# Kernel optimization log

Hardware: AMD Instinct MI355X
Metric: run time of the kernel (lower is better)

The kernel has to match this reference:

```python
import jax, jax.numpy as jnp
import numpy as np

B, DIM, F, H = 16384, 64, 8, 8
D2 = DIM // 2


def setup_inputs() -> dict:
    key = jax.random.key(0)
    ks = jax.random.split(key, 8)
    s = 0.1  # small init so exp(s_net) stays well-conditioned
    return {
        "x": jax.random.normal(ks[0], (B, DIM), jnp.float32),
        "x_star": jax.random.normal(ks[1], (B, DIM), jnp.float32),
        "W0": jax.random.normal(ks[2], (F, 4, H, D2), jnp.float32) * s,
        "b0": jax.random.normal(ks[3], (F, 4, H), jnp.float32) * s,
        "W1": jax.random.normal(ks[4], (F, 4, H, H), jnp.float32) * s,
        "b1": jax.random.normal(ks[5], (F, 4, H), jnp.float32) * s,
        "W2": jax.random.normal(ks[6], (F, 4, D2, H), jnp.float32) * s,
        "b2": jax.random.normal(ks[7], (F, 4, D2), jnp.float32) * s,
    }


def _fcnn(v, w0, c0, w1, c1, w2, c2):
    # FCNN: Linear -> Tanh -> Linear -> Tanh -> Linear, on a single vector v [D2]
    h = jnp.tanh(w0 @ v + c0)
    h = jnp.tanh(w1 @ h + c1)
    return w2 @ h + c2


def _phi(v, params):
    # Chain of n_flows RealNVP coupling layers on a single sample v [DIM].
    def step(v, p):
        W0, b0, W1, b1, W2, b2 = p  # leading axis 4 = (t1, s1, t2, s2)
        lo, up = v[:D2], v[D2:]
        t1 = _fcnn(lo, W0[0], b0[0], W1[0], b1[0], W2[0], b2[0])
        s1 = _fcnn(lo, W0[1], b0[1], W1[1], b1[1], W2[1], b2[1])
        up = t1 + up * jnp.exp(s1)
        t2 = _fcnn(up, W0[2], b0[2], W1[2], b1[2], W2[2], b2[2])
        s2 = _fcnn(up, W0[3], b0[3], W1[3], b1[3], W2[3], b2[3])
        lo = t2 + lo * jnp.exp(s2)
        return jnp.concatenate([lo, up]), None

    z, _ = jax.lax.scan(step, v, params)
    return z


def reference(x, x_star, W0, b0, W1, b1, W2, b2):
    params = (W0, b0, W1, b1, W2, b2)
    # Per-sample Jacobian of the flow (replaces torch autograd loop): [B, DIM, DIM]
    jac = jax.vmap(jax.jacfwd(lambda v: _phi(v, params)))(x)
    # -grad of quadratic potential (feature=None): -2 * (x - x_star)
    g = -2.0 * (x - x_star)
    # torch.solve(potential_grad, phi_jac): solve J u = g per sample
    return jnp.linalg.solve(jac, g[..., None])[..., 0]
```

## Files before the change

kernel.cpp:

```cpp
#include <hip/hip_runtime.h>


namespace {

typedef __fp16 f16x2 __attribute__((ext_vector_type(2)));
typedef __fp16 v4h __attribute__((ext_vector_type(4)));
typedef __fp16 v8h __attribute__((ext_vector_type(8)));
typedef float f32x4 __attribute__((ext_vector_type(4)));

constexpr int NB = 16384;

__device__ __forceinline__ float frcp(float x) { return __builtin_amdgcn_rcpf(x); }
__device__ __forceinline__ float ftanh(float x) {
  float e = __expf(2.f * x);
  return 1.f - 2.f * frcp(e + 1.f);
}
__device__ __forceinline__ f16x2 pk(float a, float b) {
  return __builtin_amdgcn_cvt_pkrtz(a, b);
}

union U8 { v8h v; f16x2 h[4]; };
union U4 { v4h v; f16x2 h[2]; };

__device__ __forceinline__ int pbase(int p) {
  return ((p >> 1) << 2) + ((p & 1) << 1);
}

template <bool JVP>
__device__ __forceinline__ void pair_apply(
    const f16x2* __restrict__ LW0, const f16x2* __restrict__ LW1,
    const f16x2* __restrict__ LW2, const float* __restrict__ LB0,
    const float* __restrict__ LB1, const float* __restrict__ LB2, int p,
    int n, int q, const float v[8], const float* __restrict__ u, float t8[8],
    float s8[8], float* __restrict__ ut8, float* __restrict__ us8) {
  v4h z4;
#pragma unroll
  for (int jj = 0; jj < 4; ++jj) z4[jj] = (__fp16)0.f;
  const f32x4 zc = {0.f, 0.f, 0.f, 0.f};

  U8 B;
  B.h[0] = pk(v[0], v[1]);
  B.h[1] = pk(v[2], v[3]);
  B.h[2] = pk(v[4], v[5]);
  B.h[3] = pk(v[6], v[7]);

  const v8h A0 = *(const v8h*)(LW0 + ((p * 64 + q * 16 + n) << 2));
  const f32x4 c0 = *(const f32x4*)(LB0 + p * 16 + q * 4);
  f32x4 d1 = __builtin_amdgcn_mfma_f32_16x16x32_f16(A0, B.v, c0, 0, 0, 0);
  float h1[4];
#pragma unroll
  for (int r = 0; r < 4; ++r) h1[r] = ftanh(d1[r]);
  U4 H1;
  H1.h[0] = pk(h1[0], h1[1]);
  H1.h[1] = pk(h1[2], h1[3]);

  const bool act1 = (n < 8) == (q < 2);
  v4h A1 = *(const v4h*)(LW1 + (p * 64 + ((n & 7) << 2) + ((q & 1) << 1) +
                                ((n >= 8) ? 32 : 0)));
  A1 = act1 ? A1 : z4;
  const f32x4 c1 = *(const f32x4*)(LB1 + p * 16 + q * 4);
  f32x4 d2 = __builtin_amdgcn_mfma_f32_16x16x16f16(A1, H1.v, c1, 0, 0, 0);
  float h2[4];
#pragma unroll
  for (int r = 0; r < 4; ++r) h2[r] = ftanh(d2[r]);
  U4 H2;
  H2.h[0] = pk(h2[0], h2[1]);
  H2.h[1] = pk(h2[2], h2[3]);

  U4 G2;
  if constexpr (JVP) {
    U8 Bu;
    Bu.h[0] = pk(u[0], u[1]);
    Bu.h[1] = pk(u[2], u[3]);
    Bu.h[2] = pk(u[4], u[5]);
    Bu.h[3] = pk(u[6], u[7]);
    f32x4 d1u = __builtin_amdgcn_mfma_f32_16x16x32_f16(A0, Bu.v, zc, 0, 0, 0);
    float g1[4];
#pragma unroll
    for (int r = 0; r < 4; ++r) g1[r] = (1.f - h1[r] * h1[r]) * d1u[r];
    U4 G1;
    G1.h[0] = pk(g1[0], g1[1]);
    G1.h[1] = pk(g1[2], g1[3]);
    f32x4 d2u = __builtin_amdgcn_mfma_f32_16x16x16f16(A1, G1.v, zc, 0, 0, 0);
    float g2[4];
#pragma unroll
    for (int r = 0; r < 4; ++r) g2[r] = (1.f - h2[r] * h2[r]) * d2u[r];
    G2.h[0] = pk(g2[0], g2[1]);
    G2.h[1] = pk(g2[2], g2[3]);
  }

#pragma unroll
  for (int b = 0; b < 4; ++b) {
    const bool act = (b < 2) == (q < 2);
    v4h Ab = *(const v4h*)(LW2 + (p * 256 + b * 64 + n * 4 + ((q & 1) << 1)));
    Ab = act ? Ab : z4;
    const f32x4 cb = *(const f32x4*)(LB2 + (p * 4 + b) * 16 + q * 4);
    f32x4 ob = __builtin_amdgcn_mfma_f32_16x16x16f16(Ab, H2.v, cb, 0, 0, 0);
    float* dst = (b < 2) ? t8 : s8;
    const int off = (b & 1) * 4;
#pragma unroll
    for (int r = 0; r < 4; ++r) dst[off + r] = ob[r];
    if constexpr (JVP) {
      f32x4 jb = __builtin_amdgcn_mfma_f32_16x16x16f16(Ab, G2.v, zc, 0, 0, 0);
      float* jdst = (b < 2) ? ut8 : us8;
#pragma unroll
      for (int r = 0; r < 4; ++r) jdst[off + r] = jb[r];
    }
  }
}

}

__global__ __launch_bounds__(256, 1) void nf_policy_kernel(
    const float* __restrict__ x, const float* __restrict__ xs,
    const float* __restrict__ gW0, const float* __restrict__ gb0,
    const float* __restrict__ gW1, const float* __restrict__ gb1,
    const float* __restrict__ gW2, const float* __restrict__ gb2,
    float* __restrict__ out) {
  __shared__ __align__(16) f16x2 LW0[4096];
  __shared__ __align__(16) f16x2 LW1[1024];
  __shared__ __align__(16) f16x2 LW2[4096];
  __shared__ __align__(16) float LB0[256];
  __shared__ __align__(16) float LB1[256];
  __shared__ __align__(16) float LB2[1024];

  const int tid = threadIdx.x;
  for (int i = tid; i < 4096; i += 256) {
    const int p = i >> 8, rem = i & 255, q = rem >> 6, rem2 = rem & 63;
    const int mm = rem2 >> 2, w = rem2 & 3;
    const int net = pbase(p) + (mm >> 3);
    const int h = mm & 7, k0 = q * 8 + w * 2;
    const float* src = gW0 + net * 256 + h * 32 + k0;
    LW0[i] = pk(src[0], src[1]);
  }
  for (int i = tid; i < 1024; i += 256) {
    const int p = i >> 6, rem = i & 63, half = rem >> 5;
    const int row = (rem >> 2) & 7, kk = rem & 3;
    const int net = pbase(p) + half;
    const float* src = gW1 + net * 64 + row * 8 + kk * 2;
    LW1[i] = pk(src[0], src[1]);
  }
  for (int i = tid; i < 4096; i += 256) {
    const int p = i >> 8, rem = i & 255, b = rem >> 6, rem2 = rem & 63;
    const int mm = rem2 >> 2, kk = rem2 & 3;
    const int net = pbase(p) + (b >> 1);
    const int d = 8 * (mm >> 2) + ((b & 1) << 2) + (mm & 3);
    const float* src = gW2 + net * 256 + d * 8 + kk * 2;
    LW2[i] = pk(src[0], src[1]);
  }
  for (int i = tid; i < 256; i += 256) {
    const int p = i >> 4, mm = i & 15;
    const int net = pbase(p) + (mm >> 3);
    LB0[i] = gb0[net * 8 + (mm & 7)];
    LB1[i] = gb1[net * 8 + (mm & 7)];
  }
  for (int i = tid; i < 1024; i += 256) {
    const int p = i >> 6, b = (i >> 4) & 3, mm = i & 15;
    const int net = pbase(p) + (b >> 1);
    const int d = 8 * (mm >> 2) + ((b & 1) << 2) + (mm & 3);
    LB2[i] = gb2[net * 32 + d];
  }
  __syncthreads();

  const int lane = tid & 63;
  const int wv = tid >> 6;
  const int n = lane & 15;
  const int q = lane >> 4;
  const int e = blockIdx.x * 64 + wv * 16 + n;

  float lo[8], up[8], av[8], bv[8];
  {
    const float* xe = x + (size_t)e * 64;
    const float* se = xs + (size_t)e * 64;
    const float4 a0 = *(const float4*)(xe + q * 8);
    const float4 a1 = *(const float4*)(xe + q * 8 + 4);
    const float4 u0 = *(const float4*)(xe + 32 + q * 8);
    const float4 u1 = *(const float4*)(xe + 32 + q * 8 + 4);
    const float4 p0 = *(const float4*)(se + q * 8);
    const float4 p1 = *(const float4*)(se + q * 8 + 4);
    const float4 r0 = *(const float4*)(se + 32 + q * 8);
    const float4 r1 = *(const float4*)(se + 32 + q * 8 + 4);
    lo[0] = a0.x; lo[1] = a0.y; lo[2] = a0.z; lo[3] = a0.w;
    lo[4] = a1.x; lo[5] = a1.y; lo[6] = a1.z; lo[7] = a1.w;
    up[0] = u0.x; up[1] = u0.y; up[2] = u0.z; up[3] = u0.w;
    up[4] = u1.x; up[5] = u1.y; up[6] = u1.z; up[7] = u1.w;
    av[0] = -2.f * (a0.x - p0.x); av[1] = -2.f * (a0.y - p0.y);
    av[2] = -2.f * (a0.z - p0.z); av[3] = -2.f * (a0.w - p0.w);
    av[4] = -2.f * (a1.x - p1.x); av[5] = -2.f * (a1.y - p1.y);
    av[6] = -2.f * (a1.z - p1.z); av[7] = -2.f * (a1.w - p1.w);
    bv[0] = -2.f * (u0.x - r0.x); bv[1] = -2.f * (u0.y - r0.y);
    bv[2] = -2.f * (u0.z - r0.z); bv[3] = -2.f * (u0.w - r0.w);
    bv[4] = -2.f * (u1.x - r1.x); bv[5] = -2.f * (u1.y - r1.y);
    bv[6] = -2.f * (u1.z - r1.z); bv[7] = -2.f * (u1.w - r1.w);
  }

  float t8[8], s8[8], ut8[8], us8[8];

#pragma unroll 1
  for (int i = 0; i < 8; ++i) {
    pair_apply<false>(LW0, LW1, LW2, LB0, LB1, LB2, 2 * i, n, q, lo, nullptr,
                      t8, s8, nullptr, nullptr);
#pragma unroll
    for (int j = 0; j < 8; ++j) up[j] = fmaf(up[j], __expf(s8[j]), t8[j]);
    pair_apply<false>(LW0, LW1, LW2, LB0, LB1, LB2, 2 * i + 1, n, q, up,
                      nullptr, t8, s8, nullptr, nullptr);
#pragma unroll
    for (int j = 0; j < 8; ++j) lo[j] = fmaf(lo[j], __expf(s8[j]), t8[j]);
  }

#pragma unroll 1
  for (int i = 7; i >= 0; --i) {
    pair_apply<true>(LW0, LW1, LW2, LB0, LB1, LB2, 2 * i + 1, n, q, up, bv,
                     t8, s8, ut8, us8);
#pragma unroll
    for (int j = 0; j < 8; ++j) {
      const float esi = __expf(-s8[j]);
      const float d = lo[j] - t8[j];
      lo[j] = d * esi;
      av[j] = (av[j] - ut8[j] - d * us8[j]) * esi;
    }
    pair_apply<true>(LW0, LW1, LW2, LB0, LB1, LB2, 2 * i, n, q, lo, av, t8,
                     s8, ut8, us8);
#pragma unroll
    for (int j = 0; j < 8; ++j) {
      const float esi = __expf(-s8[j]);
      const float d = up[j] - t8[j];
      up[j] = d * esi;
      bv[j] = (bv[j] - ut8[j] - d * us8[j]) * esi;
    }
  }

  {
    float* oe = out + (size_t)e * 64;
    float4 v;
    v.x = av[0]; v.y = av[1]; v.z = av[2]; v.w = av[3];
    *(float4*)(oe + q * 8) = v;
    v.x = av[4]; v.y = av[5]; v.z = av[6]; v.w = av[7];
    *(float4*)(oe + q * 8 + 4) = v;
    v.x = bv[0]; v.y = bv[1]; v.z = bv[2]; v.w = bv[3];
    *(float4*)(oe + 32 + q * 8) = v;
    v.x = bv[4]; v.y = bv[5]; v.z = bv[6]; v.w = bv[7];
    *(float4*)(oe + 32 + q * 8 + 4) = v;
  }
}

extern "C" void kernel_launch(void* const* d_in, const int* in_sizes, int n_in,
                              void* d_out, int out_size, void* d_ws,
                              size_t ws_size, hipStream_t stream) {
  const float* x  = (const float*)d_in[0];
  const float* xs = (const float*)d_in[1];
  const float* W0 = (const float*)d_in[2];
  const float* b0 = (const float*)d_in[3];
  const float* W1 = (const float*)d_in[4];
  const float* b1 = (const float*)d_in[5];
  const float* W2 = (const float*)d_in[6];
  const float* b2 = (const float*)d_in[7];
  float* out = (float*)d_out;

  dim3 grid(NB / 64);
  dim3 block(256);
  nf_policy_kernel<<<grid, block, 0, stream>>>(x, xs, W0, b0, W1, b1, W2, b2,
                                               out);
}
```

Baseline: 95.45 us.

## Cache forward hidden activations in LDS to skip recomputation in backward pass

```diff
diff --git a/kernel.cpp b/kernel.cpp
--- a/kernel.cpp
+++ b/kernel.cpp
@@ -19,94 +19,11 @@
   return __builtin_amdgcn_cvt_pkrtz(a, b);
 }
 
-union U8 { v8h v; f16x2 h[4]; };
-union U4 { v4h v; f16x2 h[2]; };
+union U8 { v8h v; f16x2 h[4]; float4 f4; };
+union U4 { v4h v; f16x2 h[2]; float2 f2; };
 
 __device__ __forceinline__ int pbase(int p) {
   return ((p >> 1) << 2) + ((p & 1) << 1);
-}
-
-template <bool JVP>
-__device__ __forceinline__ void pair_apply(
-    const f16x2* __restrict__ LW0, const f16x2* __restrict__ LW1,
-    const f16x2* __restrict__ LW2, const float* __restrict__ LB0,
-    const float* __restrict__ LB1, const float* __restrict__ LB2, int p,
-    int n, int q, const float v[8], const float* __restrict__ u, float t8[8],
-    float s8[8], float* __restrict__ ut8, float* __restrict__ us8) {
-  v4h z4;
-#pragma unroll
-  for (int jj = 0; jj < 4; ++jj) z4[jj] = (__fp16)0.f;
-  const f32x4 zc = {0.f, 0.f, 0.f, 0.f};
-
-  U8 B;
-  B.h[0] = pk(v[0], v[1]);
-  B.h[1] = pk(v[2], v[3]);
-  B.h[2] = pk(v[4], v[5]);
-  B.h[3] = pk(v[6], v[7]);
-
-  const v8h A0 = *(const v8h*)(LW0 + ((p * 64 + q * 16 + n) << 2));
-  const f32x4 c0 = *(const f32x4*)(LB0 + p * 16 + q * 4);
-  f32x4 d1 = __builtin_amdgcn_mfma_f32_16x16x32_f16(A0, B.v, c0, 0, 0, 0);
-  float h1[4];
-#pragma unroll
-  for (int r = 0; r < 4; ++r) h1[r] = ftanh(d1[r]);
-  U4 H1;
-  H1.h[0] = pk(h1[0], h1[1]);
-  H1.h[1] = pk(h1[2], h1[3]);
-
-  const bool act1 = (n < 8) == (q < 2);
-  v4h A1 = *(const v4h*)(LW1 + (p * 64 + ((n & 7) << 2) + ((q & 1) << 1) +
-                                ((n >= 8) ? 32 : 0)));
-  A1 = act1 ? A1 : z4;
-  const f32x4 c1 = *(const f32x4*)(LB1 + p * 16 + q * 4);
-  f32x4 d2 = __builtin_amdgcn_mfma_f32_16x16x16f16(A1, H1.v, c1, 0, 0, 0);
-  float h2[4];
-#pragma unroll
-  for (int r = 0; r < 4; ++r) h2[r] = ftanh(d2[r]);
-  U4 H2;
-  H2.h[0] = pk(h2[0], h2[1]);
-  H2.h[1] = pk(h2[2], h2[3]);
-
-  U4 G2;
-  if constexpr (JVP) {
-    U8 Bu;
-    Bu.h[0] = pk(u[0], u[1]);
-    Bu.h[1] = pk(u[2], u[3]);
-    Bu.h[2] = pk(u[4], u[5]);
-    Bu.h[3] = pk(u[6], u[7]);
-    f32x4 d1u = __builtin_amdgcn_mfma_f32_16x16x32_f16(A0, Bu.v, zc, 0, 0, 0);
-    float g1[4];
-#pragma unroll
-    for (int r = 0; r < 4; ++r) g1[r] = (1.f - h1[r] * h1[r]) * d1u[r];
-    U4 G1;
-    G1.h[0] = pk(g1[0], g1[1]);
-    G1.h[1] = pk(g1[2], g1[3]);
-    f32x4 d2u = __builtin_amdgcn_mfma_f32_16x16x16f16(A1, G1.v, zc, 0, 0, 0);
-    float g2[4];
-#pragma unroll
-    for (int r = 0; r < 4; ++r) g2[r] = (1.f - h2[r] * h2[r]) * d2u[r];
-    G2.h[0] = pk(g2[0], g2[1]);
-    G2.h[1] = pk(g2[2], g2[3]);
-  }
-
-#pragma unroll
-  for (int b = 0; b < 4; ++b) {
-    const bool act = (b < 2) == (q < 2);
-    v4h Ab = *(const v4h*)(LW2 + (p * 256 + b * 64 + n * 4 + ((q & 1) << 1)));
-    Ab = act ? Ab : z4;
-    const f32x4 cb = *(const f32x4*)(LB2 + (p * 4 + b) * 16 + q * 4);
-    f32x4 ob = __builtin_amdgcn_mfma_f32_16x16x16f16(Ab, H2.v, cb, 0, 0, 0);
-    float* dst = (b < 2) ? t8 : s8;
-    const int off = (b & 1) * 4;
-#pragma unroll
-    for (int r = 0; r < 4; ++r) dst[off + r] = ob[r];
-    if constexpr (JVP) {
-      f32x4 jb = __builtin_amdgcn_mfma_f32_16x16x16f16(Ab, G2.v, zc, 0, 0, 0);
-      float* jdst = (b < 2) ? ut8 : us8;
-#pragma unroll
-      for (int r = 0; r < 4; ++r) jdst[off + r] = jb[r];
-    }
-  }
 }
 
 }
@@ -123,13 +40,14 @@
   __shared__ __align__(16) float LB0[256];
   __shared__ __align__(16) float LB1[256];
   __shared__ __align__(16) float LB2[1024];
+  __shared__ __align__(16) float4 sHC[4096];
 
   const int tid = threadIdx.x;
   for (int i = tid; i < 4096; i += 256) {
-    const int p = i >> 8, rem = i & 255, q = rem >> 6, rem2 = rem & 63;
+    const int p = i >> 8, rem = i & 255, qq = rem >> 6, rem2 = rem & 63;
     const int mm = rem2 >> 2, w = rem2 & 3;
     const int net = pbase(p) + (mm >> 3);
-    const int h = mm & 7, k0 = q * 8 + w * 2;
+    const int h = mm & 7, k0 = qq * 8 + w * 2;
     const float* src = gW0 + net * 256 + h * 32 + k0;
     LW0[i] = pk(src[0], src[1]);
   }
@@ -167,6 +85,14 @@
   const int n = lane & 15;
   const int q = lane >> 4;
   const int e = blockIdx.x * 64 + wv * 16 + n;
+
+  v4h z4;
+#pragma unroll
+  for (int jj = 0; jj < 4; ++jj) z4[jj] = (__fp16)0.f;
+  const f32x4 zc = {0.f, 0.f, 0.f, 0.f};
+  const bool act1 = (n < 8) == (q < 2);
+  const int a1off = ((n & 7) << 2) + ((q & 1) << 1) + ((n >= 8) ? 32 : 0);
+  const int abbase = n * 4 + ((q & 1) << 1);
 
   float lo[8], up[8], av[8], bv[8];
   {
@@ -196,37 +122,124 @@
 
   float t8[8], s8[8], ut8[8], us8[8];
 
-#pragma unroll 1
-  for (int i = 0; i < 8; ++i) {
-    pair_apply<false>(LW0, LW1, LW2, LB0, LB1, LB2, 2 * i, n, q, lo, nullptr,
-                      t8, s8, nullptr, nullptr);
-#pragma unroll
-    for (int j = 0; j < 8; ++j) up[j] = fmaf(up[j], __expf(s8[j]), t8[j]);
-    pair_apply<false>(LW0, LW1, LW2, LB0, LB1, LB2, 2 * i + 1, n, q, up,
-                      nullptr, t8, s8, nullptr, nullptr);
-#pragma unroll
-    for (int j = 0; j < 8; ++j) lo[j] = fmaf(lo[j], __expf(s8[j]), t8[j]);
-  }
-
-#pragma unroll 1
-  for (int i = 7; i >= 0; --i) {
-    pair_apply<true>(LW0, LW1, LW2, LB0, LB1, LB2, 2 * i + 1, n, q, up, bv,
-                     t8, s8, ut8, us8);
+#pragma unroll
+  for (int hs = 0; hs < 16; ++hs) {
+    const int p = hs;
+    float* v = (p & 1) ? up : lo;
+    float* w = (p & 1) ? lo : up;
+    U8 B;
+    B.h[0] = pk(v[0], v[1]);
+    B.h[1] = pk(v[2], v[3]);
+    B.h[2] = pk(v[4], v[5]);
+    B.h[3] = pk(v[6], v[7]);
+    const v8h A0 = *(const v8h*)(LW0 + ((p * 64 + q * 16 + n) << 2));
+    const f32x4 c0 = *(const f32x4*)(LB0 + p * 16 + q * 4);
+    f32x4 d1 = __builtin_amdgcn_mfma_f32_16x16x32_f16(A0, B.v, c0, 0, 0, 0);
+    float h1[4];
+#pragma unroll
+    for (int r = 0; r < 4; ++r) h1[r] = ftanh(d1[r]);
+    U4 H1;
+    H1.h[0] = pk(h1[0], h1[1]);
+    H1.h[1] = pk(h1[2], h1[3]);
+    v4h A1 = *(const v4h*)(LW1 + (p * 64 + a1off));
+    A1 = act1 ? A1 : z4;
+    const f32x4 c1 = *(const f32x4*)(LB1 + p * 16 + q * 4);
+    f32x4 d2 = __builtin_amdgcn_mfma_f32_16x16x16f16(A1, H1.v, c1, 0, 0, 0);
+    float h2[4];
+#pragma unroll
+    for (int r = 0; r < 4; ++r) h2[r] = ftanh(d2[r]);
+    U4 H2;
+    H2.h[0] = pk(h2[0], h2[1]);
+    H2.h[1] = pk(h2[2], h2[3]);
+    {
+      float4 pkd;
+      pkd.x = __builtin_bit_cast(float, H1.h[0]);
+      pkd.y = __builtin_bit_cast(float, H1.h[1]);
+      pkd.z = __builtin_bit_cast(float, H2.h[0]);
+      pkd.w = __builtin_bit_cast(float, H2.h[1]);
+      sHC[p * 256 + tid] = pkd;
+    }
+#pragma unroll
+    for (int b = 0; b < 4; ++b) {
+      const bool act = (b < 2) == (q < 2);
+      v4h Ab = *(const v4h*)(LW2 + (p * 256 + b * 64 + abbase));
+      Ab = act ? Ab : z4;
+      const f32x4 cb = *(const f32x4*)(LB2 + (p * 4 + b) * 16 + q * 4);
+      f32x4 ob = __builtin_amdgcn_mfma_f32_16x16x16f16(Ab, H2.v, cb, 0, 0, 0);
+      float* dst = (b < 2) ? t8 : s8;
+      const int off = (b & 1) * 4;
+#pragma unroll
+      for (int r = 0; r < 4; ++r) dst[off + r] = ob[r];
+    }
+#pragma unroll
+    for (int j = 0; j < 8; ++j) w[j] = fmaf(w[j], __expf(s8[j]), t8[j]);
+  }
+
+#pragma unroll
+  for (int hs = 15; hs >= 0; --hs) {
+    const int p = hs;
+    float* st = (p & 1) ? lo : up;
+    float* dme = (p & 1) ? av : bv;
+    float* dot = (p & 1) ? bv : av;
+    U4 H1, H2;
+    {
+      const float4 pkd = sHC[p * 256 + tid];
+      H1.h[0] = __builtin_bit_cast(f16x2, pkd.x);
+      H1.h[1] = __builtin_bit_cast(f16x2, pkd.y);
+      H2.h[0] = __builtin_bit_cast(f16x2, pkd.z);
+      H2.h[1] = __builtin_bit_cast(f16x2, pkd.w);
+    }
+    U8 Bu;
+    Bu.h[0] = pk(dot[0], dot[1]);
+    Bu.h[1] = pk(dot[2], dot[3]);
+    Bu.h[2] = pk(dot[4], dot[5]);
+    Bu.h[3] = pk(dot[6], dot[7]);
+    const v8h A0 = *(const v8h*)(LW0 + ((p * 64 + q * 16 + n) << 2));
+    f32x4 d1u = __builtin_amdgcn_mfma_f32_16x16x32_f16(A0, Bu.v, zc, 0, 0, 0);
+    float g1[4];
+#pragma unroll
+    for (int r = 0; r < 4; ++r) {
+      const float h1r = (float)H1.v[r];
+      g1[r] = (1.f - h1r * h1r) * d1u[r];
+    }
+    U4 G1;
+    G1.h[0] = pk(g1[0], g1[1]);
+    G1.h[1] = pk(g1[2], g1[3]);
+    v4h A1 = *(const v4h*)(LW1 + (p * 64 + a1off));
+    A1 = act1 ? A1 : z4;
+    f32x4 d2u = __builtin_amdgcn_mfma_f32_16x16x16f16(A1, G1.v, zc, 0, 0, 0);
+    float g2[4];
+#pragma unroll
+    for (int r = 0; r < 4; ++r) {
+      const float h2r = (float)H2.v[r];
+      g2[r] = (1.f - h2r * h2r) * d2u[r];
+    }
+    U4 G2;
+    G2.h[0] = pk(g2[0], g2[1]);
+    G2.h[1] = pk(g2[2], g2[3]);
+#pragma unroll
+    for (int b = 0; b < 4; ++b) {
+      const bool act = (b < 2) == (q < 2);
+      v4h Ab = *(const v4h*)(LW2 + (p * 256 + b * 64 + abbase));
+      Ab = act ? Ab : z4;
+      const f32x4 cb = *(const f32x4*)(LB2 + (p * 4 + b) * 16 + q * 4);
+      f32x4 ob = __builtin_amdgcn_mfma_f32_16x16x16f16(Ab, H2.v, cb, 0, 0, 0);
+      f32x4 jb = __builtin_amdgcn_mfma_f32_16x16x16f16(Ab, G2.v, zc, 0, 0, 0);
+      float* dst = (b < 2) ? t8 : s8;
+      float* jdst = (b < 2) ? ut8 : us8;
+      const int off = (b & 1) * 4;
+#pragma unroll
+      for (int r = 0; r < 4; ++r) {
+        dst[off + r] = ob[r];
+        jdst[off + r] = jb[r];
+      }
+    }
 #pragma unroll
     for (int j = 0; j < 8; ++j) {
       const float esi = __expf(-s8[j]);
-      const float d = lo[j] - t8[j];
-      lo[j] = d * esi;
-      av[j] = (av[j] - ut8[j] - d * us8[j]) * esi;
-    }
-    pair_apply<true>(LW0, LW1, LW2, LB0, LB1, LB2, 2 * i, n, q, lo, av, t8,
-                     s8, ut8, us8);
-#pragma unroll
-    for (int j = 0; j < 8; ++j) {
-      const float esi = __expf(-s8[j]);
-      const float d = up[j] - t8[j];
-      up[j] = d * esi;
-      bv[j] = (bv[j] - ut8[j] - d * us8[j]) * esi;
+      const float d = st[j] - t8[j];
+      st[j] = d * esi;
+      dme[j] = (dme[j] - ut8[j] - d * us8[j]) * esi;
     }
   }
 
```

Result: no change. 95.42 us (-0.0%).
